# Kernel optimization log

Hardware: AMD Instinct MI355X
Metric: run time of the kernel (lower is better)

The kernel has to match this reference:

```python
import jax, jax.numpy as jnp
import numpy as np

EPS = 1e-12  # F.normalize default eps

def _l2norm(x, axis):
    n = jnp.sqrt(jnp.sum(x * x, axis=axis, keepdims=True))
    return x / jnp.maximum(n, EPS)

def setup_inputs() -> dict:
    key = jax.random.key(0)
    ks = jax.random.split(key, 6)
    N, C, K, B, OUT = 200000, 256, 64, 8, 1024
    alpha = 100.0
    feat = jax.random.normal(ks[0], (N, C), dtype=jnp.float32)
    batch_ids = jax.random.randint(ks[1], (N,), 0, B, dtype=jnp.int32)
    centroids = jax.random.uniform(ks[2], (K, C), dtype=jnp.float32)
    # _init_params: conv weight = 2*alpha*centroids, bias = -alpha*||centroid||_2
    conv_w = 2.0 * alpha * centroids
    conv_b = -alpha * jnp.sqrt(jnp.sum(centroids * centroids, axis=1))
    fc_w = jax.random.normal(ks[3], (OUT, K * C), dtype=jnp.float32) * (1.0 / np.sqrt(K * C))
    fc_b = jax.random.normal(ks[4], (OUT,), dtype=jnp.float32) * 0.01
    return {"feat": feat, "batch_ids": batch_ids, "centroids": centroids,
            "conv_w": conv_w, "conv_b": conv_b, "fc_w": fc_w, "fc_b": fc_b,
            "batch_size": B}

def reference(feat, batch_ids, centroids, conv_w, conv_b, fc_w, fc_b, batch_size):
    B = int(batch_size)
    K, C = centroids.shape
    # descriptor-wise L2 normalization (normalize_input=True)
    x = _l2norm(feat, axis=1)                       # [N, C]
    # 1x1 conv == linear: soft assignment logits per point
    logits = x @ conv_w.T + conv_b                  # [N, K]
    soft = jax.nn.softmax(logits, axis=1)           # [N, K]
    # Per-batch aggregation (replaces the python loop):
    # vlad[b,k,:] = sum_{p in b} soft[p,k] * x[p,:] - (sum_{p in b} soft[p,k]) * centroids[k,:]
    onehot = jax.nn.one_hot(batch_ids, B, dtype=x.dtype)          # [N, B]
    A = jnp.einsum('nb,nk,nc->bkc', onehot, soft, x)              # [B, K, C]
    S = jax.ops.segment_sum(soft, batch_ids, num_segments=B)      # [B, K]
    vlad = A - S[:, :, None] * centroids[None, :, :]              # [B, K, C]
    vlad = _l2norm(vlad, axis=2)                                  # intra-normalization over C
    v = vlad.reshape(B, K * C)
    out = v @ fc_w.T + fc_b                                       # [B, 1024]
    return _l2norm(out, axis=1)
```

## Files before the change

### kernel.cpp

```cpp
#include <hip/hip_runtime.h>
#include <hip/hip_bf16.h>

typedef __attribute__((ext_vector_type(8))) short bf16x8;
typedef __attribute__((ext_vector_type(4))) float f32x4;

#define PCAP 768

__device__ __forceinline__ void async_copy16(const void* g, void* l)
{
    __builtin_amdgcn_global_load_lds(
        (const __attribute__((address_space(1))) unsigned int*)g,
        (__attribute__((address_space(3))) unsigned int*)l, 16, 0, 0);
}

__global__ void p0_wsplit(const float* __restrict__ convw,
                          short* __restrict__ whi, short* __restrict__ wlo)
{
    int e = blockIdx.x * 256 + threadIdx.x;
    if (e >= 2048) return;
    int lane = e & 63;
    int kstep = (e >> 6) & 7;
    int nt = e >> 9;
    int cluster = nt * 16 + (lane & 15);
    int ch0 = kstep * 32 + (lane >> 4) * 8;
    const float* src = convw + cluster * 256 + ch0;
    #pragma unroll
    for (int j = 0; j < 8; ++j) {
        float x = src[j];
        unsigned u = __float_as_uint(x);
        unsigned uh = u & 0xffff0000u;
        float r = x - __uint_as_float(uh);
        whi[e * 8 + j] = (short)(u >> 16);
        wlo[e * 8 + j] = (short)(__float_as_uint(r) >> 16);
    }
}

__global__ __launch_bounds__(256, 3) void p1_mfma(
    const float* __restrict__ feat, const int* __restrict__ bids,
    const short* __restrict__ whi, const short* __restrict__ wlo,
    const float* __restrict__ convb,
    float* __restrict__ soft, float* __restrict__ invn, int* __restrict__ cnts, int N)
{
    __shared__ float xbuf[2][4096];
    __shared__ int cnt[8];
    const int t = threadIdx.x;
    if (t < 8) cnt[t] = 0;
    const int w = t >> 6, lane = t & 63;
    const int m = lane & 15, quad = lane >> 4;
    const int p0 = blockIdx.x * 64;

    int s_pt[4], s_inner[4];
    #pragma unroll
    for (int pass = 0; pass < 4; ++pass) {
        int slot = pass * 256 + t;
        s_pt[pass] = slot >> 4;
        s_inner[pass] = (slot & 15) ^ (s_pt[pass] & 15);
    }

    auto STAGE = [&](int bi, int ck) {
        #pragma unroll
        for (int pass = 0; pass < 4; ++pass) {
            int gpt = p0 + s_pt[pass];
            const float* src = (gpt < N)
                ? feat + (size_t)gpt * 256 + ck * 64 + s_inner[pass] * 4
                : feat;
            async_copy16(src, (char*)&xbuf[bi][0] + (size_t)(pass * 256 + w * 64) * 16);
        }
    };

    STAGE(0, 0);
    __syncthreads();

    f32x4 acc[4];
    #pragma unroll
    for (int nt = 0; nt < 4; ++nt) acc[nt] = (f32x4){0.f, 0.f, 0.f, 0.f};
    float ssq = 0.f;

    const bf16x8* WH = (const bf16x8*)whi;
    const bf16x8* WL = (const bf16x8*)wlo;
    const int ptl = w * 16 + m;

    #pragma unroll
    for (int ck = 0; ck < 4; ++ck) {
        bf16x8 wfh[2][4], wfl[2][4];
        #pragma unroll
        for (int k2 = 0; k2 < 2; ++k2)
            #pragma unroll
            for (int nt = 0; nt < 4; ++nt) {
                wfh[k2][nt] = WH[(nt * 8 + ck * 2 + k2) * 64 + lane];
                wfl[k2][nt] = WL[(nt * 8 + ck * 2 + k2) * 64 + lane];
            }
        __builtin_amdgcn_sched_barrier(0);
        if (ck < 3) STAGE((ck + 1) & 1, ck + 1);
        __builtin_amdgcn_sched_barrier(0);

        const float* B = &xbuf[ck & 1][0];
        #pragma unroll
        for (int k2 = 0; k2 < 2; ++k2) {
            int i0 = (k2 * 8 + quad * 2 + 0) ^ m;
            int i1 = (k2 * 8 + quad * 2 + 1) ^ m;
            float4 v0 = *(const float4*)(B + (ptl * 16 + i0) * 4);
            float4 v1 = *(const float4*)(B + (ptl * 16 + i1) * 4);
            float x[8] = {v0.x, v0.y, v0.z, v0.w, v1.x, v1.y, v1.z, v1.w};
            bf16x8 ahi, alo;
            #pragma unroll
            for (int j = 0; j < 8; ++j) {
                unsigned u = __float_as_uint(x[j]);
                float r = x[j] - __uint_as_float(u & 0xffff0000u);
                ahi[j] = (short)(u >> 16);
                alo[j] = (short)(__float_as_uint(r) >> 16);
                ssq += x[j] * x[j];
            }
            #pragma unroll
            for (int nt = 0; nt < 4; ++nt) {
                acc[nt] = __builtin_amdgcn_mfma_f32_16x16x32_bf16(ahi, wfh[k2][nt], acc[nt], 0, 0, 0);
                acc[nt] = __builtin_amdgcn_mfma_f32_16x16x32_bf16(ahi, wfl[k2][nt], acc[nt], 0, 0, 0);
                acc[nt] = __builtin_amdgcn_mfma_f32_16x16x32_bf16(alo, wfh[k2][nt], acc[nt], 0, 0, 0);
            }
        }
        if (ck < 3) __syncthreads();
    }

    ssq += __shfl_xor(ssq, 16);
    ssq += __shfl_xor(ssq, 32);

    float bias[4];
    #pragma unroll
    for (int nt = 0; nt < 4; ++nt) bias[nt] = convb[nt * 16 + m];

    #pragma unroll
    for (int r = 0; r < 4; ++r) {
        int pl = quad * 4 + r;
        int gpt = p0 + w * 16 + pl;
        float sq = __shfl(ssq, pl);
        float inv = rsqrtf(fmaxf(sq, 1e-24f));
        float v[4];
        #pragma unroll
        for (int nt = 0; nt < 4; ++nt) v[nt] = acc[nt][r] * inv + bias[nt];
        float mx = fmaxf(fmaxf(v[0], v[1]), fmaxf(v[2], v[3]));
        #pragma unroll
        for (int off = 8; off >= 1; off >>= 1) mx = fmaxf(mx, __shfl_xor(mx, off));
        float e[4];
        float s = 0.f;
        #pragma unroll
        for (int nt = 0; nt < 4; ++nt) { e[nt] = __expf(v[nt] - mx); s += e[nt]; }
        #pragma unroll
        for (int off = 8; off >= 1; off >>= 1) s += __shfl_xor(s, off);
        float rs = 1.0f / s;
        if (gpt < N) {
            #pragma unroll
            for (int nt = 0; nt < 4; ++nt)
                soft[(size_t)gpt * 64 + nt * 16 + m] = e[nt] * rs;
            if (m == 0) {
                invn[gpt] = inv;
                atomicAdd(&cnt[bids[gpt]], 1);
            }
        }
    }
    __syncthreads();
    if (t < 8) atomicAdd(&cnts[t], cnt[t]);
}

__global__ void p2_offsets(const int* __restrict__ cnts, int* __restrict__ offs, int* __restrict__ cur)
{
    if (threadIdx.x == 0) {
        int acc = 0;
        for (int b = 0; b < 8; ++b) { offs[b] = acc; cur[b] = acc; acc += cnts[b]; }
        offs[8] = acc;
    }
}

__global__ __launch_bounds__(256) void p2_scatter(
    const int* __restrict__ bids, int* __restrict__ cur, int* __restrict__ perm, int N)
{
    __shared__ int lcnt[8], lbase[8];
    const int t = threadIdx.x;
    if (t < 8) lcnt[t] = 0;
    __syncthreads();
    int p = blockIdx.x * 256 + t;
    int b = 0, my = 0;
    bool ok = p < N;
    if (ok) { b = bids[p]; my = atomicAdd(&lcnt[b], 1); }
    __syncthreads();
    if (t < 8) lbase[t] = atomicAdd(&cur[t], lcnt[t]);
    __syncthreads();
    if (ok) perm[lbase[b] + my] = p;
}

__global__ __launch_bounds__(256) void p3_mfma(
    const float* __restrict__ feat, const float* __restrict__ soft,
    const float* __restrict__ invn, const int* __restrict__ perm,
    const int* __restrict__ offs, float* __restrict__ partial,
    float* __restrict__ S, int split)
{
    __shared__ short xsT_hi[256 * 32];
    __shared__ short xsT_lo[256 * 32];
    __shared__ short sT_hi[64 * 32];
    __shared__ short sT_lo[64 * 32];
    __shared__ int   pidxL[PCAP];
    __shared__ float invL[PCAP];

    const int b  = blockIdx.x / split;
    const int sp = blockIdx.x % split;
    const int start = offs[b], end = offs[b + 1];
    const int len = end - start;
    const int chunk = (len + split - 1) / split;
    const int s0 = start + sp * chunk;
    int myLen = end - s0;
    myLen = max(0, min(myLen, chunk));
    myLen = min(myLen, PCAP);

    const int t = threadIdx.x;
    const int w = t >> 6, lane = t & 63;
    const int m = lane & 15, quad = lane >> 4;

    for (int i = t; i < myLen; i += 256) pidxL[i] = perm[s0 + i];
    __syncthreads();
    for (int i = t; i < myLen; i += 256) invL[i] = invn[pidxL[i]];
    __syncthreads();

    f32x4 acc[16];
    #pragma unroll
    for (int ct = 0; ct < 16; ++ct) acc[ct] = (f32x4){0.f, 0.f, 0.f, 0.f};
    float sacc = 0.f;

    const int nch = (myLen + 31) >> 5;
    for (int q = 0; q < nch; ++q) {
        const int p0 = q * 32;
        int pids[8];
        float pinv[8];
        #pragma unroll
        for (int j = 0; j < 8; ++j) {
            int pl = p0 + w * 8 + j;
            bool ok = pl < myLen;
            pids[j] = ok ? pidxL[pl] : -1;
            pinv[j] = ok ? invL[pl] : 0.f;
        }
        #pragma unroll
        for (int cg = 0; cg < 4; ++cg) {
            int c = cg * 64 + lane;
            float vals[8];
            #pragma unroll
            for (int j = 0; j < 8; ++j) {
                float v = 0.f;
                if (pids[j] >= 0) v = feat[(size_t)pids[j] * 256 + c] * pinv[j];
                vals[j] = v;
            }
            bf16x8 vh, vl;
            #pragma unroll
            for (int j = 0; j < 8; ++j) {
                unsigned u = __float_as_uint(vals[j]);
                float r = vals[j] - __uint_as_float(u & 0xffff0000u);
                vh[j] = (short)(u >> 16);
                vl[j] = (short)(__float_as_uint(r) >> 16);
            }
            *(bf16x8*)&xsT_hi[c * 32 + w * 8] = vh;
            *(bf16x8*)&xsT_lo[c * 32 + w * 8] = vl;
        }
        {
            float svals[8];
            #pragma unroll
            for (int j = 0; j < 8; ++j) {
                float v = 0.f;
                if (pids[j] >= 0) v = soft[(size_t)pids[j] * 64 + lane];
                svals[j] = v;
                sacc += v;
            }
            bf16x8 vh, vl;
            #pragma unroll
            for (int j = 0; j < 8; ++j) {
                unsigned u = __float_as_uint(svals[j]);
                float r = svals[j] - __uint_as_float(u & 0xffff0000u);
                vh[j] = (short)(u >> 16);
                vl[j] = (short)(__float_as_uint(r) >> 16);
            }
            *(bf16x8*)&sT_hi[lane * 32 + w * 8] = vh;
            *(bf16x8*)&sT_lo[lane * 32 + w * 8] = vl;
        }
        __syncthreads();
        bf16x8 ah = *(const bf16x8*)&sT_hi[(w * 16 + m) * 32 + quad * 8];
        bf16x8 al = *(const bf16x8*)&sT_lo[(w * 16 + m) * 32 + quad * 8];
        #pragma unroll
        for (int ct = 0; ct < 16; ++ct) {
            bf16x8 bh = *(const bf16x8*)&xsT_hi[(ct * 16 + m) * 32 + quad * 8];
            bf16x8 bl = *(const bf16x8*)&xsT_lo[(ct * 16 + m) * 32 + quad * 8];
            acc[ct] = __builtin_amdgcn_mfma_f32_16x16x32_bf16(ah, bh, acc[ct], 0, 0, 0);
            acc[ct] = __builtin_amdgcn_mfma_f32_16x16x32_bf16(ah, bl, acc[ct], 0, 0, 0);
            acc[ct] = __builtin_amdgcn_mfma_f32_16x16x32_bf16(al, bh, acc[ct], 0, 0, 0);
        }
        __syncthreads();
    }

    float* dst = partial + (size_t)(b * split + sp) * 64 * 256;
    #pragma unroll
    for (int ct = 0; ct < 16; ++ct) {
        #pragma unroll
        for (int r = 0; r < 4; ++r) {
            int k = w * 16 + quad * 4 + r;
            dst[k * 256 + ct * 16 + m] = acc[ct][r];
        }
    }
    atomicAdd(S + b * 64 + lane, sacc);
}

__global__ __launch_bounds__(256) void p4a_vlad(
    const float* __restrict__ partial, const float* __restrict__ S,
    const float* __restrict__ cents, float* __restrict__ v, int split)
{
    const int b = blockIdx.x >> 6, k = blockIdx.x & 63;
    const int t = threadIdx.x;
    float sum = 0.f;
    const float* base = partial + ((size_t)(b * split) * 64 + k) * 256 + t;
    for (int sp = 0; sp < split; ++sp)
        sum += base[(size_t)sp * 64 * 256];
    float val = sum - S[b * 64 + k] * cents[k * 256 + t];
    float sq = val * val;
    #pragma unroll
    for (int off = 32; off >= 1; off >>= 1) sq += __shfl_xor(sq, off);
    __shared__ float wsum[4];
    if ((t & 63) == 0) wsum[t >> 6] = sq;
    __syncthreads();
    float tot = wsum[0] + wsum[1] + wsum[2] + wsum[3];
    float r = 1.0f / fmaxf(sqrtf(tot), 1e-12f);
    v[b * 16384 + k * 256 + t] = val * r;
}

__global__ __launch_bounds__(256) void p4b_fc(
    const float* __restrict__ v, const float* __restrict__ fcw,
    const float* __restrict__ fcb, float* __restrict__ pre)
{
    const int t = threadIdx.x;
    const int o0 = blockIdx.x * 4;
    float acc[4][8] = {};
    for (int it = 0; it < 64; ++it) {
        int i = it * 256 + t;
        float wv[4];
        #pragma unroll
        for (int oo = 0; oo < 4; ++oo) wv[oo] = fcw[(size_t)(o0 + oo) * 16384 + i];
        #pragma unroll
        for (int b = 0; b < 8; ++b) {
            float vv = v[b * 16384 + i];
            #pragma unroll
            for (int oo = 0; oo < 4; ++oo) acc[oo][b] += wv[oo] * vv;
        }
    }
    __shared__ float red[32][4];
    #pragma unroll
    for (int oo = 0; oo < 4; ++oo)
        #pragma unroll
        for (int b = 0; b < 8; ++b) {
            float sv = acc[oo][b];
            #pragma unroll
            for (int off = 32; off >= 1; off >>= 1) sv += __shfl_xor(sv, off);
            if ((t & 63) == 0) red[oo * 8 + b][t >> 6] = sv;
        }
    __syncthreads();
    if (t < 32) {
        int oo = t >> 3, b = t & 7;
        float sv = red[t][0] + red[t][1] + red[t][2] + red[t][3];
        pre[b * 1024 + o0 + oo] = sv + fcb[o0 + oo];
    }
}

__global__ __launch_bounds__(256) void p5_norm(const float* __restrict__ pre, float* __restrict__ out)
{
    const int b = blockIdx.x, t = threadIdx.x;
    float vals[4];
    float sq = 0.f;
    #pragma unroll
    for (int i = 0; i < 4; ++i) {
        vals[i] = pre[b * 1024 + t + 256 * i];
        sq += vals[i] * vals[i];
    }
    #pragma unroll
    for (int off = 32; off >= 1; off >>= 1) sq += __shfl_xor(sq, off);
    __shared__ float wsum[4];
    if ((t & 63) == 0) wsum[t >> 6] = sq;
    __syncthreads();
    float tot = wsum[0] + wsum[1] + wsum[2] + wsum[3];
    float r = 1.0f / fmaxf(sqrtf(tot), 1e-12f);
    #pragma unroll
    for (int i = 0; i < 4; ++i) out[b * 1024 + t + 256 * i] = vals[i] * r;
}

extern "C" void kernel_launch(void* const* d_in, const int* in_sizes, int n_in,
                              void* d_out, int out_size, void* d_ws, size_t ws_size,
                              hipStream_t stream)
{
    const float* feat  = (const float*)d_in[0];
    const int*   bids  = (const int*)d_in[1];
    const float* cents = (const float*)d_in[2];
    const float* convw = (const float*)d_in[3];
    const float* convb = (const float*)d_in[4];
    const float* fcw   = (const float*)d_in[5];
    const float* fcb   = (const float*)d_in[6];
    float* out = (float*)d_out;

    const int N = in_sizes[0] / 256;

    const size_t base_floats = 16384
                             + (size_t)N * 64  + N
                             + 512  + 8 * 16384  + 8192 ;
    const size_t base_ints = (size_t)N + 8 + 9 + 8;
    int split = 96;
    while (split > 16) {
        size_t tot = (base_floats + (size_t)split * 8 * 16384) * 4 + base_ints * 4;
        if (tot <= ws_size) break;
        split -= 16;
    }

    short* whi = (short*)d_ws;
    short* wlo = whi + 16384;
    float* soft = (float*)(wlo + 16384);
    float* invn = soft + (size_t)N * 64;
    float* partial = invn + N;
    float* S    = partial + (size_t)split * 8 * 16384;
    float* v    = S + 512;
    float* pre  = v + 8 * 16384;
    int* perm = (int*)(pre + 8192);
    int* cnts = perm + N;
    int* offs = cnts + 8;
    int* cur  = offs + 9;

    hipMemsetAsync(S, 0, 512 * sizeof(float), stream);
    hipMemsetAsync(cnts, 0, 8 * sizeof(int), stream);

    p0_wsplit<<<8, 256, 0, stream>>>(convw, whi, wlo);
    p1_mfma<<<(N + 63) / 64, 256, 0, stream>>>(feat, bids, whi, wlo, convb, soft, invn, cnts, N);
    p2_offsets<<<1, 64, 0, stream>>>(cnts, offs, cur);
    p2_scatter<<<(N + 255) / 256, 256, 0, stream>>>(bids, cur, perm, N);
    p3_mfma<<<8 * split, 256, 0, stream>>>(feat, soft, invn, perm, offs, partial, S, split);
    p4a_vlad<<<512, 256, 0, stream>>>(partial, S, cents, v, split);
    p4b_fc<<<256, 256, 0, stream>>>(v, fcw, fcb, pre);
    p5_norm<<<8, 256, 0, stream>>>(pre, out);
}
```

Baseline: 549.2 us.

## Prefetch next chunk into registers, XOR-swizzle LDS tiles, set occupancy bound in p3_mfma

```diff
diff --git a/kernel.cpp b/kernel.cpp
--- a/kernel.cpp
+++ b/kernel.cpp
@@ -187,7 +187,7 @@
     if (ok) perm[lbase[b] + my] = p;
 }
 
-__global__ __launch_bounds__(256) void p3_mfma(
+__global__ __launch_bounds__(256, 2) void p3_mfma(
     const float* __restrict__ feat, const float* __restrict__ soft,
     const float* __restrict__ invn, const int* __restrict__ perm,
     const int* __restrict__ offs, float* __restrict__ partial,
@@ -225,10 +225,14 @@
     float sacc = 0.f;
 
     const int nch = (myLen + 31) >> 5;
-    for (int q = 0; q < nch; ++q) {
+
+    int   pids[8];
+    float pinv[8];
+    float xv[4][8];
+    float sv[8];
+
+    auto FETCH = [&](int q) {
         const int p0 = q * 32;
-        int pids[8];
-        float pinv[8];
         #pragma unroll
         for (int j = 0; j < 8; ++j) {
             int pl = p0 + w * 8 + j;
@@ -239,56 +243,68 @@
         #pragma unroll
         for (int cg = 0; cg < 4; ++cg) {
             int c = cg * 64 + lane;
-            float vals[8];
+            #pragma unroll
+            for (int j = 0; j < 8; ++j)
+                xv[cg][j] = (pids[j] >= 0) ? feat[(size_t)pids[j] * 256 + c] : 0.f;
+        }
+        #pragma unroll
+        for (int j = 0; j < 8; ++j)
+            sv[j] = (pids[j] >= 0) ? soft[(size_t)pids[j] * 64 + lane] : 0.f;
+    };
+
+    if (nch > 0) FETCH(0);
+
+    for (int q = 0; q < nch; ++q) {
+        __syncthreads();
+        #pragma unroll
+        for (int cg = 0; cg < 4; ++cg) {
+            int c = cg * 64 + lane;
+            bf16x8 vh, vl;
             #pragma unroll
             for (int j = 0; j < 8; ++j) {
-                float v = 0.f;
-                if (pids[j] >= 0) v = feat[(size_t)pids[j] * 256 + c] * pinv[j];
-                vals[j] = v;
-            }
-            bf16x8 vh, vl;
-            #pragma unroll
-            for (int j = 0; j < 8; ++j) {
-                unsigned u = __float_as_uint(vals[j]);
-                float r = vals[j] - __uint_as_float(u & 0xffff0000u);
+                float v = xv[cg][j] * pinv[j];
+                unsigned u = __float_as_uint(v);
+                float r = v - __uint_as_float(u & 0xffff0000u);
                 vh[j] = (short)(u >> 16);
                 vl[j] = (short)(__float_as_uint(r) >> 16);
             }
-            *(bf16x8*)&xsT_hi[c * 32 + w * 8] = vh;
-            *(bf16x8*)&xsT_lo[c * 32 + w * 8] = vl;
+            int slot = (w ^ (c & 3)) * 8;
+            *(bf16x8*)&xsT_hi[c * 32 + slot] = vh;
+            *(bf16x8*)&xsT_lo[c * 32 + slot] = vl;
         }
         {
-            float svals[8];
+            bf16x8 vh, vl;
             #pragma unroll
             for (int j = 0; j < 8; ++j) {
-                float v = 0.f;
-                if (pids[j] >= 0) v = soft[(size_t)pids[j] * 64 + lane];
-                svals[j] = v;
+                float v = sv[j];
                 sacc += v;
-            }
-            bf16x8 vh, vl;
-            #pragma unroll
-            for (int j = 0; j < 8; ++j) {
-                unsigned u = __float_as_uint(svals[j]);
-                float r = svals[j] - __uint_as_float(u & 0xffff0000u);
+                unsigned u = __float_as_uint(v);
+                float r = v - __uint_as_float(u & 0xffff0000u);
                 vh[j] = (short)(u >> 16);
                 vl[j] = (short)(__float_as_uint(r) >> 16);
             }
-            *(bf16x8*)&sT_hi[lane * 32 + w * 8] = vh;
-            *(bf16x8*)&sT_lo[lane * 32 + w * 8] = vl;
-        }
+            int slot = (w ^ (lane & 3)) * 8;
+            *(bf16x8*)&sT_hi[lane * 32 + slot] = vh;
+            *(bf16x8*)&sT_lo[lane * 32 + slot] = vl;
+        }
+        if (q + 1 < nch) FETCH(q + 1);
         __syncthreads();
-        bf16x8 ah = *(const bf16x8*)&sT_hi[(w * 16 + m) * 32 + quad * 8];
-        bf16x8 al = *(const bf16x8*)&sT_lo[(w * 16 + m) * 32 + quad * 8];
-        #pragma unroll
-        for (int ct = 0; ct < 16; ++ct) {
-            bf16x8 bh = *(const bf16x8*)&xsT_hi[(ct * 16 + m) * 32 + quad * 8];
-            bf16x8 bl = *(const bf16x8*)&xsT_lo[(ct * 16 + m) * 32 + quad * 8];
-            acc[ct] = __builtin_amdgcn_mfma_f32_16x16x32_bf16(ah, bh, acc[ct], 0, 0, 0);
-            acc[ct] = __builtin_amdgcn_mfma_f32_16x16x32_bf16(ah, bl, acc[ct], 0, 0, 0);
-            acc[ct] = __builtin_amdgcn_mfma_f32_16x16x32_bf16(al, bh, acc[ct], 0, 0, 0);
-        }
-        __syncthreads();
+        {
+            const int arow = w * 16 + m;
+            const int aslot = (quad ^ (m & 3)) * 8;
+            bf16x8 ah = *(const bf16x8*)&sT_hi[arow * 32 + aslot];
+            bf16x8 al = *(const bf16x8*)&sT_lo[arow * 32 + aslot];
+            const int bslot = (quad ^ (m & 3)) * 8;
+            #pragma unroll
+            for (int ct = 0; ct < 16; ++ct) {
+                const int brow = ct * 16 + m;
+                bf16x8 bh = *(const bf16x8*)&xsT_hi[brow * 32 + bslot];
+                bf16x8 bl = *(const bf16x8*)&xsT_lo[brow * 32 + bslot];
+                acc[ct] = __builtin_amdgcn_mfma_f32_16x16x32_bf16(ah, bh, acc[ct], 0, 0, 0);
+                acc[ct] = __builtin_amdgcn_mfma_f32_16x16x32_bf16(ah, bl, acc[ct], 0, 0, 0);
+                acc[ct] = __builtin_amdgcn_mfma_f32_16x16x32_bf16(al, bh, acc[ct], 0, 0, 0);
+            }
+        }
     }
 
     float* dst = partial + (size_t)(b * split + sp) * 64 * 256;
```

Measured after the change: 481.0 us. 1.14x faster.
